# Kernel optimization log

Hardware: AMD Instinct MI355X
Metric: run time of the kernel (lower is better)

Reference implementation:

```python
import jax, jax.numpy as jnp
import numpy as np

B, M, L, D, H, DFF, K, NL = 32, 512, 512, 128, 8, 256, 16, 2


def setup_inputs() -> dict:
    key = jax.random.key(0)
    ks = jax.random.split(key, 12)
    s = 0.02
    p = lambda i, shape: (jax.random.normal(ks[i], shape, jnp.float32) * s)
    return {
        "enc_out_vari": jax.random.normal(ks[0], (B, M, D), jnp.float32),
        "x_enc": jax.random.normal(ks[1], (B, L, M), jnp.float32),
        "conv1_W": p(2, (D, D)), "conv1_b": jnp.zeros((D,), jnp.float32),
        "conv2_W": p(3, (D, D)), "conv2_b": jnp.zeros((D,), jnp.float32),
        "Wq": p(4, (NL, D, D)), "Wk": p(5, (NL, D, D)),
        "Wv": p(6, (NL, D, D)), "Wo": p(7, (NL, D, D)),
        "ffn_W1": p(8, (NL, D, DFF)), "ffn_b1": jnp.zeros((NL, DFF), jnp.float32),
        "ffn_W2": p(9, (NL, DFF, D)), "ffn_b2": jnp.zeros((NL, D), jnp.float32),
        "ln1_g": jnp.ones((NL, D), jnp.float32), "ln1_b": jnp.zeros((NL, D), jnp.float32),
        "ln2_g": jnp.ones((NL, D), jnp.float32), "ln2_b": jnp.zeros((NL, D), jnp.float32),
    }


def _ln(x, g, b, eps=1e-5):
    mu = x.mean(-1, keepdims=True)
    var = ((x - mu) ** 2).mean(-1, keepdims=True)
    return (x - mu) * jax.lax.rsqrt(var + eps) * g + b


def _gcn_conv(x, src, dst, W, b, N):
    # PyG GCNConv: XW, add self loops, symmetric D^-1/2 (A+I) D^-1/2 aggregation, + bias
    h = x @ W
    loop = jnp.arange(N)
    s = jnp.concatenate([src, loop])
    d = jnp.concatenate([dst, loop])
    deg = jax.ops.segment_sum(jnp.ones_like(d, jnp.float32), d, num_segments=N)
    dinv = jnp.where(deg > 0, jax.lax.rsqrt(deg), 0.0)
    norm = dinv[s] * dinv[d]
    out = jax.ops.segment_sum(h[s] * norm[:, None], d, num_segments=N)
    return out + b


def _forward(enc_out_vari, x_enc, conv1_W, conv1_b, conv2_W, conv2_b,
             Wq, Wk, Wv, Wo, ffn_W1, ffn_b1, ffn_W2, ffn_b2,
             ln1_g, ln1_b, ln2_g, ln2_b):
    # --- dynamic graph from Pearson correlation (faithful: ascending argsort, idx 1..k) ---
    x = x_enc.transpose(0, 2, 1)                      # [B, M, L]
    c = x - x.mean(-1, keepdims=True)
    cov = jnp.einsum('bml,bnl->bmn', c, c) / (L - 1)  # [B, M, M]
    std = jnp.sqrt(jnp.diagonal(cov, axis1=-2, axis2=-1))
    std = jnp.where(std == 0, 1.0, std)
    corr = cov / (std[:, :, None] * std[:, None, :])
    neighbors = jnp.argsort(corr, axis=-1)[:, :, 1:K + 1]  # [B, M, K]
    row = jnp.tile(jnp.arange(M), K)                  # arange(M).repeat(k) in torch
    col = neighbors.reshape(B, M * K)
    offs = (jnp.arange(B) * M)[:, None]               # batch the graphs into one
    src = (row[None, :] + offs).reshape(-1)
    dst = (col + offs).reshape(-1)
    N = B * M
    # --- 2-layer GCN over flattened node set ---
    x_raw = enc_out_vari.reshape(N, D)
    h1 = jax.nn.relu(_gcn_conv(x_raw, src, dst, conv1_W, conv1_b, N))
    h2 = jax.nn.relu(_gcn_conv(h1, src, dst, conv2_W, conv2_b, N))
    xg = h2.reshape(B, M, D)
    # --- cross-attention transformer encoder: query stream = enc_out_vari, kv = GCN output ---
    h = enc_out_vari
    hd = D // H
    scale = 1.0 / jnp.sqrt(jnp.float32(hd))
    for l in range(NL):
        q = (h @ Wq[l]).reshape(B, M, H, hd)
        k_ = (xg @ Wk[l]).reshape(B, M, H, hd)
        v = (xg @ Wv[l]).reshape(B, M, H, hd)
        att = jax.nn.softmax(jnp.einsum('bqhd,bkhd->bhqk', q, k_) * scale, axis=-1)
        o = jnp.einsum('bhqk,bkhd->bqhd', att, v).reshape(B, M, D) @ Wo[l]
        h = _ln(h + o, ln1_g[l], ln1_b[l])
        f = jax.nn.relu(h @ ffn_W1[l] + ffn_b1[l]) @ ffn_W2[l] + ffn_b2[l]
        h = _ln(h + f, ln2_g[l], ln2_b[l])
    return h


def reference(enc_out_vari, x_enc, conv1_W, conv1_b, conv2_W, conv2_b,
              Wq, Wk, Wv, Wo, ffn_W1, ffn_b1, ffn_W2, ffn_b2,
              ln1_g, ln1_b, ln2_g, ln2_b):
    return _forward(enc_out_vari, x_enc, conv1_W, conv1_b, conv2_W, conv2_b,
                    Wq, Wk, Wv, Wo, ffn_W1, ffn_b1, ffn_W2, ffn_b2,
                    ln1_g, ln1_b, ln2_g, ln2_b)
```

## Files before the change

kernel.cpp:

```cpp
#include <hip/hip_runtime.h>
#include <float.h>

#define BB 32
#define MMv 512
#define LLv 512
#define DDv 128
#define HHv 8
#define DFFv 256
#define KNB 16
#define NLAY 2
#define NNODE (BB*MMv)
#define TOTE  (NNODE*KNB)
#define WTOT  294912

typedef unsigned short ushort_t;
typedef unsigned int u32;
typedef __attribute__((ext_vector_type(8))) short bf16x8;
typedef __attribute__((ext_vector_type(4))) float f32x4;

__device__ __forceinline__ float bf2f(ushort_t u){
  union { u32 i; float f; } x; x.i = ((u32)u) << 16; return x.f;
}
__device__ __forceinline__ ushort_t f2bf(float f){
  union { u32 i; float f; } x; x.f = f;
  u32 r = x.i + 0x7FFFu + ((x.i >> 16) & 1u);
  return (ushort_t)(r >> 16);
}
__device__ __forceinline__ float ldx(const void* p, size_t i, int f32){
  return f32 ? ((const float*)p)[i] : bf2f(((const ushort_t*)p)[i]);
}
__device__ __forceinline__ float wsum(float v){
  #pragma unroll
  for(int s=32;s;s>>=1) v += __shfl_xor(v,s);
  return v;
}

__global__ __launch_bounds__(256) void diag_fill_k(float* out, int n, float val){
  for(int i = blockIdx.x*256 + threadIdx.x; i < n; i += gridDim.x*256) out[i] = val;
}

struct P18 { const ushort_t* p[18]; int n[18]; };
__global__ __launch_bounds__(256) void ddet_k(P18 a, int* DF){
  int i = blockIdx.x;
  const ushort_t* q = a.p[i];
  int P = min(a.n[i], 4096);
  int t = threadIdx.x;
  int r1 = 0, evenNZ = 0, oddNZ = 0;
  for(int j=t; j<P; j+=256){
    ushort_t v = q[j];
    if(((v >> 7) & 0xFF) >= 0xC0) r1 = 1;
    if(v){ if(j & 1) oddNZ = 1; else evenNZ = 1; }
  }
  __shared__ int sh[3];
  if(t==0){ sh[0]=0; sh[1]=0; sh[2]=0; }
  __syncthreads();
  if(r1) atomicOr(&sh[0],1);
  if(evenNZ) atomicOr(&sh[1],1);
  if(oddNZ) atomicOr(&sh[2],1);
  __syncthreads();
  if(t==0) DF[i] = sh[0] | ((sh[1]==0) & (sh[2]!=0));
}

__global__ __launch_bounds__(256) void prep_k(const void* c1W, const void* c2W,
    const void* Wq, const void* Wk, const void* Wv, const void* Wo,
    const void* W1, const void* W2, ushort_t* Wth, ushort_t* Wtl, const int* DF){
  __shared__ ushort_t th[32][33];
  __shared__ ushort_t tl[32][33];
  int job = blockIdx.z;
  const void* src; int dfi; size_t soff, doff; int K, N;
  switch(job){
    case 0:  src=c1W; dfi=2;  soff=0; K=128; N=128; doff=0; break;
    case 1:  src=c2W; dfi=4;  soff=0; K=128; N=128; doff=16384; break;
    case 2: case 3:
      src=Wq; dfi=6; soff=(size_t)(job-2)*16384; K=128; N=128;
      doff=32768 + (size_t)(job-2)*49152; break;
    case 4: case 5:
      src=Wk; dfi=7; soff=(size_t)(job-4)*16384; K=128; N=128;
      doff=32768 + (size_t)(job-4)*49152 + 16384; break;
    case 6: case 7:
      src=Wv; dfi=8; soff=(size_t)(job-6)*16384; K=128; N=128;
      doff=32768 + (size_t)(job-6)*49152 + 32768; break;
    case 8: case 9:
      src=Wo; dfi=9; soff=(size_t)(job-8)*16384; K=128; N=128;
      doff=131072 + (size_t)(job-8)*16384; break;
    case 10: case 11:
      src=W1; dfi=10; soff=(size_t)(job-10)*32768; K=128; N=256;
      doff=163840 + (size_t)(job-10)*32768; break;
    default:
      src=W2; dfi=12; soff=(size_t)(job-12)*32768; K=256; N=128;
      doff=229376 + (size_t)(job-12)*32768; break;
  }
  int n0 = blockIdx.x*32, k0 = blockIdx.y*32;
  if(n0 >= N || k0 >= K) return;
  int f32 = DF[dfi];
  int tx = threadIdx.x, ty = threadIdx.y;
  #pragma unroll
  for(int i=0;i<4;i++){
    int k = k0+ty+8*i, n = n0+tx;
    float x = ldx(src, soff + (size_t)k*N + n, f32);
    ushort_t hi = f2bf(x);
    ushort_t lo = f2bf(x - bf2f(hi));
    th[ty+8*i][tx] = hi; tl[ty+8*i][tx] = lo;
  }
  __syncthreads();
  #pragma unroll
  for(int i=0;i<4;i++){
    int n = n0+ty+8*i, k = k0+tx;
    size_t d = doff + (size_t)n*K + k;
    Wth[d] = th[tx][ty+8*i];
    Wtl[d] = tl[tx][ty+8*i];
  }
}

__global__ __launch_bounds__(256) void split_k(const void* xe, ushort_t* Xhi,
                                               ushort_t* Xlo, const int* DF){
  __shared__ ushort_t th[32][33];
  __shared__ ushort_t tl[32][33];
  int f32 = DF[1];
  int b = blockIdx.z;
  int m0 = blockIdx.x*32, l0 = blockIdx.y*32;
  int tx = threadIdx.x, ty = threadIdx.y;
  #pragma unroll
  for(int i=0;i<4;i++){
    int l = l0+ty+8*i, m = m0+tx;
    float x = ldx(xe, (size_t)b*LLv*MMv + (size_t)l*MMv + m, f32);
    ushort_t hi = f2bf(x);
    ushort_t lo = f2bf(x - bf2f(hi));
    th[ty+8*i][tx] = hi; tl[ty+8*i][tx] = lo;
  }
  __syncthreads();
  #pragma unroll
  for(int i=0;i<4;i++){
    size_t d = (size_t)b*MMv*LLv + (size_t)(m0+ty+8*i)*LLv + l0+tx;
    Xhi[d] = th[tx][ty+8*i];
    Xlo[d] = tl[tx][ty+8*i];
  }
}

__global__ __launch_bounds__(256) void stats2_k(const ushort_t* Xhi, const ushort_t* Xlo,
                                                double* S64, double* R64){
  int row = blockIdx.x*4 + (threadIdx.x >> 6);
  int lane = threadIdx.x & 63;
  const ushort_t* Hr = Xhi + (size_t)row*LLv + lane*8;
  const ushort_t* Lr = Xlo + (size_t)row*LLv + lane*8;
  float s = 0.f, ss = 0.f;
  #pragma unroll
  for(int j=0;j<8;j++){
    float x = bf2f(Hr[j]) + bf2f(Lr[j]);
    s += x; ss = fmaf(x, x, ss);
  }
  s = wsum(s); ss = wsum(ss);
  if(lane == 0){
    S64[row] = (double)s;
    float cov = (ss - s*s*(1.0f/LLv)) * (1.0f/(LLv-1));
    float sd = (cov > 0.f) ? sqrtf(cov) : 0.f;
    R64[row] = (sd > 0.f) ? (double)(1.0f/sd) : 1.0;
  }
}

__global__ __launch_bounds__(1024) void corrsel_k(const ushort_t* Xhi, const ushort_t* Xlo,
                                                  const double* S64, const double* R64,
                                                  int* nbr, const int* DF){
  __shared__ __attribute__((aligned(16))) ushort_t Ah[32*520];
  __shared__ __attribute__((aligned(16))) ushort_t Al[32*520];
  __shared__ float Cs[32*516];
  int f32 = DF[1];
  int lin = blockIdx.y*16 + blockIdx.x;
  int xcd = lin & 7, slot = lin >> 3;
  int b = xcd + 8*(slot >> 4);
  int strip = slot & 15;
  int m0 = strip*32;
  int t = threadIdx.x;
  int wave = t >> 6, lane = t & 63;
  int quad = lane >> 4, l16 = lane & 15;
  const ushort_t* Hb = Xhi + (size_t)b*MMv*LLv;
  const ushort_t* Lb = Xlo + (size_t)b*MMv*LLv;
  for(int idx=t; idx<2048; idx+=1024){
    int mm = idx >> 6, c8 = (idx & 63)*8;
    *(bf16x8*)&Ah[mm*520 + c8] = *(const bf16x8*)&Hb[(size_t)(m0+mm)*LLv + c8];
    *(bf16x8*)&Al[mm*520 + c8] = *(const bf16x8*)&Lb[(size_t)(m0+mm)*LLv + c8];
  }
  __syncthreads();
  const double* Sb = S64 + b*MMv;
  const double* Rb = R64 + b*MMv;
  int nbase = wave*32;
  for(int cs=0; cs<2; cs++){
    int nn = nbase + cs*16 + l16;
    size_t brow = (size_t)nn*LLv + quad*8;
    f32x4 a00={0.f,0.f,0.f,0.f}, a01={0.f,0.f,0.f,0.f}, a02={0.f,0.f,0.f,0.f};
    f32x4 a10={0.f,0.f,0.f,0.f}, a11={0.f,0.f,0.f,0.f}, a12={0.f,0.f,0.f,0.f};
    if(f32){
      #pragma unroll
      for(int g=0; g<4; g++){
        bf16x8 bh[4], bl[4];
        #pragma unroll
        for(int j=0;j<4;j++) bh[j] = *(const bf16x8*)&Hb[brow + g*128 + j*32];
        #pragma unroll
        for(int j=0;j<4;j++) bl[j] = *(const bf16x8*)&Lb[brow + g*128 + j*32];
        #pragma unroll
        for(int j=0;j<4;j++){
          int ko = g*128 + j*32 + quad*8;
          bf16x8 ah0 = *(const bf16x8*)&Ah[l16*520 + ko];
          bf16x8 al0 = *(const bf16x8*)&Al[l16*520 + ko];
          bf16x8 ah1 = *(const bf16x8*)&Ah[(16+l16)*520 + ko];
          bf16x8 al1 = *(const bf16x8*)&Al[(16+l16)*520 + ko];
          a00 = __builtin_amdgcn_mfma_f32_16x16x32_bf16(ah0, bh[j], a00, 0, 0, 0);
          a01 = __builtin_amdgcn_mfma_f32_16x16x32_bf16(ah0, bl[j], a01, 0, 0, 0);
          a02 = __builtin_amdgcn_mfma_f32_16x16x32_bf16(al0, bh[j], a02, 0, 0, 0);
          a10 = __builtin_amdgcn_mfma_f32_16x16x32_bf16(ah1, bh[j], a10, 0, 0, 0);
          a11 = __builtin_amdgcn_mfma_f32_16x16x32_bf16(ah1, bl[j], a11, 0, 0, 0);
          a12 = __builtin_amdgcn_mfma_f32_16x16x32_bf16(al1, bh[j], a12, 0, 0, 0);
        }
      }
    } else {
      #pragma unroll
      for(int g=0; g<2; g++){
        bf16x8 bh[8];
        #pragma unroll
        for(int j=0;j<8;j++) bh[j] = *(const bf16x8*)&Hb[brow + g*256 + j*32];
        #pragma unroll
        for(int j=0;j<8;j++){
          int ko = g*256 + j*32 + quad*8;
          bf16x8 ah0 = *(const bf16x8*)&Ah[l16*520 + ko];
          bf16x8 ah1 = *(const bf16x8*)&Ah[(16+l16)*520 + ko];
          if(j & 1){
            a01 = __builtin_amdgcn_mfma_f32_16x16x32_bf16(ah0, bh[j], a01, 0, 0, 0);
            a11 = __builtin_amdgcn_mfma_f32_16x16x32_bf16(ah1, bh[j], a11, 0, 0, 0);
          } else {
            a00 = __builtin_amdgcn_mfma_f32_16x16x32_bf16(ah0, bh[j], a00, 0, 0, 0);
            a10 = __builtin_amdgcn_mfma_f32_16x16x32_bf16(ah1, bh[j], a10, 0, 0, 0);
          }
        }
      }
    }
    float sn = (float)(Sb[nn]*(1.0/LLv));
    float rn = (float)Rb[nn];
    #pragma unroll
    for(int r=0;r<4;r++){
      int ml0 = quad*4 + r;
      float s0 = a00[r] + a01[r] + a02[r];
      float cov0 = (s0 - (float)Sb[m0+ml0]*sn) * (1.0f/(LLv-1));
      Cs[ml0*516 + nn] = cov0 * (float)Rb[m0+ml0] * rn;
      int ml1 = 16 + ml0;
      float s1 = a10[r] + a11[r] + a12[r];
      float cov1 = (s1 - (float)Sb[m0+ml1]*sn) * (1.0f/(LLv-1));
      Cs[ml1*516 + nn] = cov1 * (float)Rb[m0+ml1] * rn;
    }
  }
  __syncthreads();
  for(int rr=0; rr<2; rr++){
    int r = wave*2 + rr;
    float vals[8];
    #pragma unroll
    for(int j=0;j<8;j++) vals[j] = Cs[r*516 + lane + 64*j];
    for(int it=0; it<=KNB; it++){
      float bvv = FLT_MAX; int bi = 0x7fffffff;
      #pragma unroll
      for(int j=0;j<8;j++){
        int n = lane + 64*j;
        if(vals[j] < bvv){ bvv = vals[j]; bi = n; }
      }
      #pragma unroll
      for(int s=32; s; s>>=1){
        float v2 = __shfl_xor(bvv, s);
        int   i2 = __shfl_xor(bi,  s);
        if(v2 < bvv || (v2 == bvv && i2 < bi)){ bvv = v2; bi = i2; }
      }
      int gbi = bi;
      int bic = min(max(gbi, 0), MMv-1);
      if(it > 0 && lane == 0) nbr[(size_t)(b*MMv + m0 + r)*KNB + it-1] = bic;
      if((gbi & 63) == lane && gbi < MMv){
        int jj = gbi >> 6;
        #pragma unroll
        for(int j=0;j<8;j++) if(j == jj) vals[j] = FLT_MAX;
      }
    }
  }
}

__global__ __launch_bounds__(256) void zero_k(int* p){
  p[blockIdx.x*256 + threadIdx.x] = 0;
}

__global__ __launch_bounds__(256) void hist_k(const int* nbr, int* cnt){
  int tid = blockIdx.x*256 + threadIdx.x;
  int b = tid >> 13;
  int col = min(max(nbr[tid], 0), MMv-1);
  atomicAdd(&cnt[b*MMv + col], 1);
}

__global__ __launch_bounds__(256) void scan_k(const int* cnt, int* off,
                                              int* cursor, float* dinv){
  __shared__ int part[256];
  int t = threadIdx.x;
  int base = t*64, s = 0;
  for(int i=0;i<64;i++) s += cnt[base+i];
  part[t] = s; __syncthreads();
  for(int st=1; st<256; st<<=1){
    int v = (t >= st) ? part[t-st] : 0;
    __syncthreads();
    part[t] += v; __syncthreads();
  }
  int run = (t > 0) ? part[t-1] : 0;
  for(int i=0;i<64;i++){
    int idx = base+i;
    off[idx] = run; cursor[idx] = run;
    run += cnt[idx];
    dinv[idx] = 1.0f/sqrtf((float)(cnt[idx]+1));
  }
  if(t == 255) off[NNODE] = run;
}

__global__ __launch_bounds__(256) void fill_k(const int* nbr, int* cursor, int* esrc){
  int tid = blockIdx.x*256 + threadIdx.x;
  int b = tid >> 13;
  int rem = tid & 8191;
  int col = min(max(nbr[tid], 0), MMv-1);
  int dst = b*MMv + col;
  int srcl = rem & 511;
  int pos = atomicAdd(&cursor[dst], 1);
  pos = min(max(pos, 0), TOTE-1);
  esrc[pos] = b*MMv + srcl;
}

__global__ __launch_bounds__(256) void gemm_k(const float* A,
                                              const ushort_t* Wth, const ushort_t* Wtl,
                                              size_t woffT, int wdi,
                                              const void* bias, int boff, int bdi,
                                              float* C, int Kd, int Dout, int relu,
                                              const int* DF){
  __shared__ __attribute__((aligned(16))) ushort_t Ah[64*72];
  __shared__ __attribute__((aligned(16))) ushort_t Al[64*72];
  __shared__ __attribute__((aligned(16))) ushort_t Wh[32*72];
  __shared__ __attribute__((aligned(16))) ushort_t Wl[32*72];
  int wf32 = DF[wdi];
  int bf32 = DF[bdi];
  int m0 = blockIdx.y*64, n0 = blockIdx.x*32;
  int t = threadIdx.x;
  int wave = t >> 6, lane = t & 63;
  int quad = lane >> 4, l16 = lane & 15;
  f32x4 acc[2];
  #pragma unroll
  for(int nt=0;nt<2;nt++) acc[nt] = (f32x4){0.f,0.f,0.f,0.f};
  for(int kc=0; kc<Kd; kc+=64){
    for(int s=t; s<1024; s+=256){
      int row = s >> 4, c4 = (s & 15)*4;
      float4 av = *(const float4*)&A[(size_t)(m0+row)*Kd + kc + c4];
      ushort_t h0=f2bf(av.x), h1=f2bf(av.y), h2=f2bf(av.z), h3=f2bf(av.w);
      ushort_t g0=f2bf(av.x-bf2f(h0)), g1=f2bf(av.y-bf2f(h1));
      ushort_t g2=f2bf(av.z-bf2f(h2)), g3=f2bf(av.w-bf2f(h3));
      *(ushort4*)&Ah[row*72 + c4] = make_ushort4(h0,h1,h2,h3);
      *(ushort4*)&Al[row*72 + c4] = make_ushort4(g0,g1,g2,g3);
    }
    for(int s=t; s<256; s+=256){
      int row = s >> 3, c8 = (s & 7)*8;
      size_t g = woffT + (size_t)(n0+row)*Kd + kc + c8;
      *(bf16x8*)&Wh[row*72 + c8] = *(const bf16x8*)&Wth[g];
      if(wf32) *(bf16x8*)&Wl[row*72 + c8] = *(const bf16x8*)&Wtl[g];
    }
    __syncthreads();
    #pragma unroll
    for(int kk=0; kk<64; kk+=32){
      int ko = kk + quad*8;
      bf16x8 ah = *(const bf16x8*)&Ah[(wave*16+l16)*72 + ko];
      bf16x8 al = *(const bf16x8*)&Al[(wave*16+l16)*72 + ko];
      #pragma unroll
      for(int nt=0; nt<2; nt++){
        bf16x8 wh = *(const bf16x8*)&Wh[(nt*16+l16)*72 + ko];
        acc[nt] = __builtin_amdgcn_mfma_f32_16x16x32_bf16(ah, wh, acc[nt], 0, 0, 0);
        acc[nt] = __builtin_amdgcn_mfma_f32_16x16x32_bf16(al, wh, acc[nt], 0, 0, 0);
        if(wf32){
          bf16x8 wl = *(const bf16x8*)&Wl[(nt*16+l16)*72 + ko];
          acc[nt] = __builtin_amdgcn_mfma_f32_16x16x32_bf16(ah, wl, acc[nt], 0, 0, 0);
        }
      }
    }
    __syncthreads();
  }
  #pragma unroll
  for(int nt=0; nt<2; nt++){
    int n = n0 + nt*16 + l16;
    float bv = bias ? ldx(bias, boff + n, bf32) : 0.f;
    #pragma unroll
    for(int r=0; r<2*2; r++){
      float v = acc[nt][r] + bv;
      if(relu) v = fmaxf(v, 0.f);
      C[(size_t)(m0 + wave*16 + quad*4 + r)*Dout + n] = v;
    }
  }
}

__global__ __launch_bounds__(256) void qkv_k(const float* hF, const float* xg,
                                             const ushort_t* Wth, const ushort_t* Wtl,
                                             size_t qoff, float* t0, float* kv,
                                             const int* DF){
  __shared__ __attribute__((aligned(16))) ushort_t Ah[64*72];
  __shared__ __attribute__((aligned(16))) ushort_t Al[64*72];
  __shared__ __attribute__((aligned(16))) ushort_t Wh[32*72];
  __shared__ __attribute__((aligned(16))) ushort_t Wl[32*72];
  int m0 = blockIdx.y*64, n0 = blockIdx.x*32;
  int wdi = (n0 < 128) ? 6 : ((n0 < 256) ? 7 : 8);
  int wf32 = DF[wdi];
  const float* A = (n0 < 128) ? hF : xg;
  int t = threadIdx.x;
  int wave = t >> 6, lane = t & 63;
  int quad = lane >> 4, l16 = lane & 15;
  f32x4 acc[2];
  #pragma unroll
  for(int nt=0;nt<2;nt++) acc[nt] = (f32x4){0.f,0.f,0.f,0.f};
  for(int kc=0; kc<DDv; kc+=64){
    for(int s=t; s<1024; s+=256){
      int row = s >> 4, c4 = (s & 15)*4;
      float4 av = *(const float4*)&A[(size_t)(m0+row)*DDv + kc + c4];
      ushort_t h0=f2bf(av.x), h1=f2bf(av.y), h2=f2bf(av.z), h3=f2bf(av.w);
      ushort_t g0=f2bf(av.x-bf2f(h0)), g1=f2bf(av.y-bf2f(h1));
      ushort_t g2=f2bf(av.z-bf2f(h2)), g3=f2bf(av.w-bf2f(h3));
      *(ushort4*)&Ah[row*72 + c4] = make_ushort4(h0,h1,h2,h3);
      *(ushort4*)&Al[row*72 + c4] = make_ushort4(g0,g1,g2,g3);
    }
    for(int s=t; s<256; s+=256){
      int row = s >> 3, c8 = (s & 7)*8;
      size_t g = qoff + (size_t)(n0+row)*DDv + kc + c8;
      *(bf16x8*)&Wh[row*72 + c8] = *(const bf16x8*)&Wth[g];
      if(wf32) *(bf16x8*)&Wl[row*72 + c8] = *(const bf16x8*)&Wtl[g];
    }
    __syncthreads();
    #pragma unroll
    for(int kk=0; kk<64; kk+=32){
      int ko = kk + quad*8;
      bf16x8 ah = *(const bf16x8*)&Ah[(wave*16+l16)*72 + ko];
      bf16x8 al = *(const bf16x8*)&Al[(wave*16+l16)*72 + ko];
      #pragma unroll
      for(int nt=0; nt<2; nt++){
        bf16x8 wh = *(const bf16x8*)&Wh[(nt*16+l16)*72 + ko];
        acc[nt] = __builtin_amdgcn_mfma_f32_16x16x32_bf16(ah, wh, acc[nt], 0, 0, 0);
        acc[nt] = __builtin_amdgcn_mfma_f32_16x16x32_bf16(al, wh, acc[nt], 0, 0, 0);
        if(wf32){
          bf16x8 wl = *(const bf16x8*)&Wl[(nt*16+l16)*72 + ko];
          acc[nt] = __builtin_amdgcn_mfma_f32_16x16x32_bf16(ah, wl, acc[nt], 0, 0, 0);
        }
      }
    }
    __syncthreads();
  }
  float* C = (n0 < 128) ? t0 : kv;
  int ldC = (n0 < 128) ? 128 : 256;
  int nb  = (n0 < 128) ? n0 : (n0 - 128);
  #pragma unroll
  for(int nt=0; nt<2; nt++){
    int n = nb + nt*16 + l16;
    #pragma unroll
    for(int r=0; r<4; r++){
      C[(size_t)(m0 + wave*16 + quad*4 + r)*ldC + n] = acc[nt][r];
    }
  }
}

__global__ __launch_bounds__(256) void agg_k(const float* xw, const int* off,
                                             const int* esrc, const float* dinv,
                                             const void* bias, int bdi, float* out,
                                             const int* DF){
  int f32 = DF[bdi];
  int node = blockIdx.x*4 + (threadIdx.x >> 6);
  int lane = threadIdx.x & 63;
  float dn = dinv[node];
  float2 xv = ((const float2*)(xw + (size_t)node*DDv))[lane];
  float a0 = dn*dn*xv.x;
  float a1 = dn*dn*xv.y;
  int e0 = min(max(off[node], 0), TOTE);
  int e1 = min(max(off[node+1], e0), TOTE);
  int e = e0;
  for(; e + 4 <= e1; e += 4){
    int s0 = min(max(esrc[e+0], 0), NNODE-1);
    int s1 = min(max(esrc[e+1], 0), NNODE-1);
    int s2 = min(max(esrc[e+2], 0), NNODE-1);
    int s3 = min(max(esrc[e+3], 0), NNODE-1);
    float2 v0 = ((const float2*)(xw + (size_t)s0*DDv))[lane];
    float2 v1 = ((const float2*)(xw + (size_t)s1*DDv))[lane];
    float2 v2 = ((const float2*)(xw + (size_t)s2*DDv))[lane];
    float2 v3 = ((const float2*)(xw + (size_t)s3*DDv))[lane];
    float w0 = dinv[s0]*dn, w1 = dinv[s1]*dn, w2 = dinv[s2]*dn, w3 = dinv[s3]*dn;
    a0 = fmaf(w0, v0.x, a0); a1 = fmaf(w0, v0.y, a1);
    a0 = fmaf(w1, v1.x, a0); a1 = fmaf(w1, v1.y, a1);
    a0 = fmaf(w2, v2.x, a0); a1 = fmaf(w2, v2.y, a1);
    a0 = fmaf(w3, v3.x, a0); a1 = fmaf(w3, v3.y, a1);
  }
  for(; e < e1; e++){
    int s = min(max(esrc[e], 0), NNODE-1);
    float w = dinv[s]*dn;
    float2 sv = ((const float2*)(xw + (size_t)s*DDv))[lane];
    a0 = fmaf(w, sv.x, a0);
    a1 = fmaf(w, sv.y, a1);
  }
  a0 += ldx(bias, 2*lane, f32); a1 += ldx(bias, 2*lane+1, f32);
  ((float2*)(out + (size_t)node*DDv))[lane] = make_float2(fmaxf(a0,0.f), fmaxf(a1,0.f));
}

__global__ __launch_bounds__(1024) void attn_k(const float* qg, const float* kv,
                                               float* og){
  __shared__ float Ks[512*16];
  __shared__ float Vs[512*16];
  int bh = blockIdx.x;
  int b = bh >> 3, hh = bh & 7;
  size_t baseq = (size_t)b*MMv*DDv + (size_t)hh*16;
  size_t basekv = (size_t)b*MMv*256 + (size_t)hh*16;
  int t = threadIdx.x;
  for(int idx=t; idx<2048; idx+=1024){
    int kk = idx >> 2, i4 = (idx & 3)*4;
    ((float4*)Ks)[idx] = *(const float4*)&kv[basekv + (size_t)kk*256 + i4];
    ((float4*)Vs)[idx] = *(const float4*)&kv[basekv + (size_t)kk*256 + 128 + i4];
  }
  __syncthreads();
  int r = t & 511, g = t >> 9;
  float qr[16];
  #pragma unroll
  for(int i4=0;i4<4;i4++){
    float4 qv = *(const float4*)&qg[baseq + (size_t)r*DDv + i4*4];
    qr[i4*4+0]=qv.x; qr[i4*4+1]=qv.y; qr[i4*4+2]=qv.z; qr[i4*4+3]=qv.w;
  }
  float m = -FLT_MAX, l = 0.f;
  float acc[16] = {};
  int k0 = g*256;
  for(int kk=k0; kk<k0+256; kk++){
    const float* kp = &Ks[kk*16];
    float s = 0.f;
    #pragma unroll
    for(int i=0;i<16;i++) s = fmaf(qr[i], kp[i], s);
    s *= 0.25f;
    if(s > m){
      float c = __expf(m - s);
      l *= c;
      #pragma unroll
      for(int i=0;i<16;i++) acc[i] *= c;
      m = s;
    }
    float p = __expf(s - m);
    l += p;
    const float* vp = &Vs[kk*16];
    #pragma unroll
    for(int i=0;i<16;i++) acc[i] = fmaf(p, vp[i], acc[i]);
  }
  __syncthreads();
  if(g == 1){
    #pragma unroll
    for(int i=0;i<16;i++) Ks[r*16 + i] = acc[i];
    Vs[r] = m; Vs[512 + r] = l;
  }
  __syncthreads();
  if(g == 0){
    float m1 = Vs[r], l1 = Vs[512 + r];
    float M = fmaxf(m, m1);
    float c0 = __expf(m - M), c1 = __expf(m1 - M);
    float inv = 1.0f/(l*c0 + l1*c1);
    #pragma unroll
    for(int i=0;i<16;i++)
      og[baseq + (size_t)r*DDv + i] = (acc[i]*c0 + Ks[r*16 + i]*c1)*inv;
  }
}

__global__ __launch_bounds__(256) void ln_k(const float* h, const float* delta,
                                            const void* g, int gdi, const void* bb, int bdi, int po,
                                            float* dst, const int* DF){
  int gf32 = DF[gdi], bf32 = DF[bdi];
  int row = blockIdx.x*4 + (threadIdx.x >> 6);
  int lane = threadIdx.x & 63;
  const float2* hr = (const float2*)(h + (size_t)row*DDv);
  const float2* dr = (const float2*)(delta + (size_t)row*DDv);
  float2 hv = hr[lane], dv = dr[lane];
  float x0 = hv.x + dv.x, x1 = hv.y + dv.y;
  float mu = wsum(x0 + x1) * (1.0f/DDv);
  float d0 = x0 - mu, d1 = x1 - mu;
  float var = wsum(d0*d0 + d1*d1) * (1.0f/DDv);
  float rs = 1.0f/sqrtf(var + 1e-5f);
  int c0 = lane*2;
  float y0 = d0*rs*ldx(g, po+c0,   gf32) + ldx(bb, po+c0,   bf32);
  float y1 = d1*rs*ldx(g, po+c0+1, gf32) + ldx(bb, po+c0+1, bf32);
  ((float2*)(dst + (size_t)row*DDv))[lane] = make_float2(y0, y1);
}

__global__ __launch_bounds__(256) void cvt_k(const void* in, float* out, const int* DF){
  int f32 = DF[0];
  int tid = blockIdx.x*256 + threadIdx.x;
  out[tid] = ldx(in, tid, f32);
}

extern "C" void kernel_launch(void* const* d_in, const int* in_sizes, int n_in,
                              void* d_out, int out_size, void* d_ws, size_t ws_size,
                              hipStream_t stream) {
  if(n_in != 18){
    diag_fill_k<<<256, 256, 0, stream>>>((float*)d_out, out_size, 1000.0f);
    return;
  }
  const int expect[18] = {
    BB*MMv*DDv, BB*LLv*MMv, DDv*DDv, DDv, DDv*DDv, DDv,
    NLAY*DDv*DDv, NLAY*DDv*DDv, NLAY*DDv*DDv, NLAY*DDv*DDv,
    NLAY*DDv*DFFv, NLAY*DFFv, NLAY*DFFv*DDv, NLAY*DDv,
    NLAY*DDv, NLAY*DDv, NLAY*DDv, NLAY*DDv
  };
  for(int i=0;i<18;i++){
    if(in_sizes[i] != expect[i]){
      diag_fill_k<<<256, 256, 0, stream>>>((float*)d_out, out_size, 2000.0f + 10.0f*i);
      return;
    }
  }

  const void* enc  = d_in[0];
  const void* xe   = d_in[1];
  const void* c1W  = d_in[2];
  const void* c1b  = d_in[3];
  const void* c2W  = d_in[4];
  const void* c2b  = d_in[5];
  const void* Wq   = d_in[6];
  const void* Wk   = d_in[7];
  const void* Wv   = d_in[8];
  const void* Wo   = d_in[9];
  const void* W1   = d_in[10];
  const void* b1   = d_in[11];
  const void* W2   = d_in[12];
  const void* b2   = d_in[13];
  const void* ln1g = d_in[14];
  const void* ln1b = d_in[15];
  const void* ln2g = d_in[16];
  const void* ln2b = d_in[17];

  char* ws = (char*)d_ws;
  size_t o = 0;
  auto alloc = [&](size_t bytes){ size_t r = o; o = (o + bytes + 255) & ~(size_t)255; return r; };
  double* S64  = (double*)(ws + alloc((size_t)NNODE*8));
  double* R64  = (double*)(ws + alloc((size_t)NNODE*8));
  float* dinv  = (float*)(ws + alloc((size_t)NNODE*4));
  int*   cnt   = (int*)  (ws + alloc((size_t)NNODE*4));
  int*   cursor= (int*)  (ws + alloc((size_t)NNODE*4));
  int*   off   = (int*)  (ws + alloc((size_t)(NNODE+1)*4));
  int*   nbr   = (int*)  (ws + alloc((size_t)TOTE*4));
  int*   esrc  = (int*)  (ws + alloc((size_t)TOTE*4));
  int*   DF    = (int*)  (ws + alloc(256));
  ushort_t* Wth = (ushort_t*)(ws + alloc((size_t)WTOT*2));
  ushort_t* Wtl = (ushort_t*)(ws + alloc((size_t)WTOT*2));
  const size_t ACTF = (size_t)NNODE*DDv*4;
  float* hF = (float*)(ws + alloc(ACTF));
  float* xg = (float*)(ws + alloc(ACTF));
  float* t0 = (float*)(ws + alloc(ACTF));
  float* t1 = (float*)(ws + alloc(ACTF));
  float* t2 = (float*)(ws + alloc(ACTF));
  float* t3 = (float*)(ws + alloc(ACTF));
  float* kv = t1;
  float* fb = t1;
  ushort_t* Xhi = (ushort_t*)hF;
  ushort_t* Xlo = Xhi + (size_t)BB*MMv*LLv;
  if(ws_size < o){
    diag_fill_k<<<256, 256, 0, stream>>>((float*)d_out, out_size, 3000.0f);
    return;
  }

  P18 pack;
  for(int i=0;i<18;i++){ pack.p[i] = (const ushort_t*)d_in[i]; pack.n[i] = in_sizes[i]; }
  ddet_k<<<18, 256, 0, stream>>>(pack, DF);
  prep_k<<<dim3(8,8,14), dim3(32,8), 0, stream>>>(c1W, c2W, Wq, Wk, Wv, Wo, W1, W2,
                                                  Wth, Wtl, DF);

  split_k<<<dim3(16,16,BB), dim3(32,8), 0, stream>>>(xe, Xhi, Xlo, DF);
  stats2_k<<<NNODE/4, 256, 0, stream>>>(Xhi, Xlo, S64, R64);
  corrsel_k<<<dim3(16, BB), 1024, 0, stream>>>(Xhi, Xlo, S64, R64, nbr, DF);
  zero_k<<<NNODE/256, 256, 0, stream>>>(cnt);
  hist_k<<<TOTE/256, 256, 0, stream>>>(nbr, cnt);
  scan_k<<<1, 256, 0, stream>>>(cnt, off, cursor, dinv);
  fill_k<<<TOTE/256, 256, 0, stream>>>(nbr, cursor, esrc);

  cvt_k<<<NNODE*DDv/256, 256, 0, stream>>>(enc, hF, DF);
  gemm_k<<<dim3(4,256), 256, 0, stream>>>(hF, Wth, Wtl, 0, 2, nullptr, 0, 3, t0, DDv, DDv, 0, DF);
  agg_k<<<NNODE/4, 256, 0, stream>>>(t0, off, esrc, dinv, c1b, 3, t1, DF);
  gemm_k<<<dim3(4,256), 256, 0, stream>>>(t1, Wth, Wtl, 16384, 4, nullptr, 0, 5, t0, DDv, DDv, 0, DF);
  agg_k<<<NNODE/4, 256, 0, stream>>>(t0, off, esrc, dinv, c2b, 5, xg, DF);

  for(int l=0; l<NLAY; l++){
    qkv_k<<<dim3(12,256), 256, 0, stream>>>(hF, xg, Wth, Wtl,
                                            32768 + (size_t)l*49152, t0, kv, DF);
    attn_k<<<BB*HHv, 1024, 0, stream>>>(t0, kv, t3);
    gemm_k<<<dim3(4,256), 256, 0, stream>>>(t3, Wth, Wtl, 131072 + (size_t)l*16384, 9, nullptr, 0, 9, t0, DDv, DDv, 0, DF);
    ln_k<<<NNODE/4, 256, 0, stream>>>(hF, t0, ln1g, 14, ln1b, 15, l*DDv, hF, DF);
    gemm_k<<<dim3(8,256), 256, 0, stream>>>(hF, Wth, Wtl, 163840 + (size_t)l*32768, 10, b1, l*DFFv, 11, fb, DDv, DFFv, 1, DF);
    gemm_k<<<dim3(4,256), 256, 0, stream>>>(fb, Wth, Wtl, 229376 + (size_t)l*32768, 12, b2, l*DDv, 13, t0, DFFv, DDv, 0, DF);
    float* dst = (l == NLAY-1) ? (float*)d_out : hF;
    ln_k<<<NNODE/4, 256, 0, stream>>>(hF, t0, ln2g, 16, ln2b, 17, l*DDv, dst, DF);
  }
}
```

Before: 730.0 us.

## Alias correlation shared buffers and cut accumulators in corrsel kernel

```diff
diff --git a/kernel.cpp b/kernel.cpp
--- a/kernel.cpp
+++ b/kernel.cpp
@@ -158,12 +158,13 @@
   }
 }
 
-__global__ __launch_bounds__(1024) void corrsel_k(const ushort_t* Xhi, const ushort_t* Xlo,
-                                                  const double* S64, const double* R64,
-                                                  int* nbr, const int* DF){
-  __shared__ __attribute__((aligned(16))) ushort_t Ah[32*520];
-  __shared__ __attribute__((aligned(16))) ushort_t Al[32*520];
-  __shared__ float Cs[32*516];
+__global__ __launch_bounds__(1024, 8) void corrsel_k(const ushort_t* Xhi, const ushort_t* Xlo,
+                                                     const double* S64, const double* R64,
+                                                     int* nbr, const int* DF){
+  __shared__ __attribute__((aligned(16))) char smem[66560];
+  ushort_t* Ah = (ushort_t*)smem;
+  ushort_t* Al = Ah + 32*520;
+  float*    Cs = (float*)smem;
   int f32 = DF[1];
   int lin = blockIdx.y*16 + blockIdx.x;
   int xcd = lin & 7, slot = lin >> 3;
@@ -184,67 +185,74 @@
   const double* Sb = S64 + b*MMv;
   const double* Rb = R64 + b*MMv;
   int nbase = wave*32;
+  float corr[16];
+  int nnv[2];
+  #pragma unroll
   for(int cs=0; cs<2; cs++){
     int nn = nbase + cs*16 + l16;
+    nnv[cs] = nn;
     size_t brow = (size_t)nn*LLv + quad*8;
-    f32x4 a00={0.f,0.f,0.f,0.f}, a01={0.f,0.f,0.f,0.f}, a02={0.f,0.f,0.f,0.f};
-    f32x4 a10={0.f,0.f,0.f,0.f}, a11={0.f,0.f,0.f,0.f}, a12={0.f,0.f,0.f,0.f};
+    f32x4 acc0 = {0.f,0.f,0.f,0.f};
+    f32x4 acc1 = {0.f,0.f,0.f,0.f};
     if(f32){
       #pragma unroll
+      for(int g=0; g<8; g++){
+        bf16x8 bh[2], bl[2];
+        #pragma unroll
+        for(int j=0;j<2;j++) bh[j] = *(const bf16x8*)&Hb[brow + g*64 + j*32];
+        #pragma unroll
+        for(int j=0;j<2;j++) bl[j] = *(const bf16x8*)&Lb[brow + g*64 + j*32];
+        #pragma unroll
+        for(int j=0;j<2;j++){
+          int ko = g*64 + j*32 + quad*8;
+          bf16x8 ah0 = *(const bf16x8*)&Ah[l16*520 + ko];
+          bf16x8 al0 = *(const bf16x8*)&Al[l16*520 + ko];
+          bf16x8 ah1 = *(const bf16x8*)&Ah[(16+l16)*520 + ko];
+          bf16x8 al1 = *(const bf16x8*)&Al[(16+l16)*520 + ko];
+          acc0 = __builtin_amdgcn_mfma_f32_16x16x32_bf16(ah0, bh[j], acc0, 0, 0, 0);
+          acc0 = __builtin_amdgcn_mfma_f32_16x16x32_bf16(ah0, bl[j], acc0, 0, 0, 0);
+          acc0 = __builtin_amdgcn_mfma_f32_16x16x32_bf16(al0, bh[j], acc0, 0, 0, 0);
+          acc1 = __builtin_amdgcn_mfma_f32_16x16x32_bf16(ah1, bh[j], acc1, 0, 0, 0);
+          acc1 = __builtin_amdgcn_mfma_f32_16x16x32_bf16(ah1, bl[j], acc1, 0, 0, 0);
+          acc1 = __builtin_amdgcn_mfma_f32_16x16x32_bf16(al1, bh[j], acc1, 0, 0, 0);
+        }
+      }
+    } else {
+      #pragma unroll
       for(int g=0; g<4; g++){
-        bf16x8 bh[4], bl[4];
+        bf16x8 bh[4];
         #pragma unroll
         for(int j=0;j<4;j++) bh[j] = *(const bf16x8*)&Hb[brow + g*128 + j*32];
-        #pragma unroll
-        for(int j=0;j<4;j++) bl[j] = *(const bf16x8*)&Lb[brow + g*128 + j*32];
         #pragma unroll
         for(int j=0;j<4;j++){
           int ko = g*128 + j*32 + quad*8;
           bf16x8 ah0 = *(const bf16x8*)&Ah[l16*520 + ko];
-          bf16x8 al0 = *(const bf16x8*)&Al[l16*520 + ko];
           bf16x8 ah1 = *(const bf16x8*)&Ah[(16+l16)*520 + ko];
-          bf16x8 al1 = *(const bf16x8*)&Al[(16+l16)*520 + ko];
-          a00 = __builtin_amdgcn_mfma_f32_16x16x32_bf16(ah0, bh[j], a00, 0, 0, 0);
-          a01 = __builtin_amdgcn_mfma_f32_16x16x32_bf16(ah0, bl[j], a01, 0, 0, 0);
-          a02 = __builtin_amdgcn_mfma_f32_16x16x32_bf16(al0, bh[j], a02, 0, 0, 0);
-          a10 = __builtin_amdgcn_mfma_f32_16x16x32_bf16(ah1, bh[j], a10, 0, 0, 0);
-          a11 = __builtin_amdgcn_mfma_f32_16x16x32_bf16(ah1, bl[j], a11, 0, 0, 0);
-          a12 = __builtin_amdgcn_mfma_f32_16x16x32_bf16(al1, bh[j], a12, 0, 0, 0);
+          acc0 = __builtin_amdgcn_mfma_f32_16x16x32_bf16(ah0, bh[j], acc0, 0, 0, 0);
+          acc1 = __builtin_amdgcn_mfma_f32_16x16x32_bf16(ah1, bh[j], acc1, 0, 0, 0);
         }
       }
-    } else {
-      #pragma unroll
-      for(int g=0; g<2; g++){
-        bf16x8 bh[8];
-        #pragma unroll
-        for(int j=0;j<8;j++) bh[j] = *(const bf16x8*)&Hb[brow + g*256 + j*32];
-        #pragma unroll
-        for(int j=0;j<8;j++){
-          int ko = g*256 + j*32 + quad*8;
-          bf16x8 ah0 = *(const bf16x8*)&Ah[l16*520 + ko];
-          bf16x8 ah1 = *(const bf16x8*)&Ah[(16+l16)*520 + ko];
-          if(j & 1){
-            a01 = __builtin_amdgcn_mfma_f32_16x16x32_bf16(ah0, bh[j], a01, 0, 0, 0);
-            a11 = __builtin_amdgcn_mfma_f32_16x16x32_bf16(ah1, bh[j], a11, 0, 0, 0);
-          } else {
-            a00 = __builtin_amdgcn_mfma_f32_16x16x32_bf16(ah0, bh[j], a00, 0, 0, 0);
-            a10 = __builtin_amdgcn_mfma_f32_16x16x32_bf16(ah1, bh[j], a10, 0, 0, 0);
-          }
-        }
-      }
     }
     float sn = (float)(Sb[nn]*(1.0/LLv));
     float rn = (float)Rb[nn];
     #pragma unroll
     for(int r=0;r<4;r++){
       int ml0 = quad*4 + r;
-      float s0 = a00[r] + a01[r] + a02[r];
-      float cov0 = (s0 - (float)Sb[m0+ml0]*sn) * (1.0f/(LLv-1));
-      Cs[ml0*516 + nn] = cov0 * (float)Rb[m0+ml0] * rn;
+      float cov0 = (acc0[r] - (float)Sb[m0+ml0]*sn) * (1.0f/(LLv-1));
+      corr[cs*8 + r] = cov0 * (float)Rb[m0+ml0] * rn;
       int ml1 = 16 + ml0;
-      float s1 = a10[r] + a11[r] + a12[r];
-      float cov1 = (s1 - (float)Sb[m0+ml1]*sn) * (1.0f/(LLv-1));
-      Cs[ml1*516 + nn] = cov1 * (float)Rb[m0+ml1] * rn;
+      float cov1 = (acc1[r] - (float)Sb[m0+ml1]*sn) * (1.0f/(LLv-1));
+      corr[cs*8 + 4 + r] = cov1 * (float)Rb[m0+ml1] * rn;
+    }
+  }
+  __syncthreads();
+  #pragma unroll
+  for(int cs=0; cs<2; cs++){
+    #pragma unroll
+    for(int r=0;r<4;r++){
+      int ml0 = quad*4 + r;
+      Cs[ml0*516 + nnv[cs]] = corr[cs*8 + r];
+      Cs[(16+ml0)*516 + nnv[cs]] = corr[cs*8 + 4 + r];
     }
   }
   __syncthreads();
```

Result: no change. 717.4 us (-1.7%).
